# Optimization experiments

Hardware: AMD Instinct MI355X
Metric: run time of the kernel (lower is better)

Reference implementation:

```python
import jax, jax.numpy as jnp
import numpy as np

ALPHA = 4.0  # spikingjelly sigmoid surrogate alpha
EPS = 1e-5   # BatchNorm eps
TAU = 2.0
NUM_HEADS = 8

@jax.custom_vjp
def _spike(x):
    return (x >= 0.0).astype(x.dtype)

def _spike_fwd(x):
    return _spike(x), x

def _spike_bwd(x, g):
    s = jax.nn.sigmoid(ALPHA * x)
    return (g * ALPHA * s * (1.0 - s),)

_spike.defvjp(_spike_fwd, _spike_bwd)

def lif(x, v_th=1.0):
    # MultiStepLIFNode: v += (x - v)/tau, spike = H(v - v_th), hard reset to 0 (detached)
    def step(v, xt):
        v = v + (xt - v) / TAU
        s = _spike(v - v_th)
        v = v * (1.0 - jax.lax.stop_gradient(s))
        return v, s
    _, spikes = jax.lax.scan(step, jnp.zeros_like(x[0]), x)
    return spikes

def bn(x, gamma, beta, mean, var):
    sh = (1, 1, -1, 1, 1)  # channel axis 2 of [T,B,C,H,W]
    inv = gamma.reshape(sh) / jnp.sqrt(var.reshape(sh) + EPS)
    return (x - mean.reshape(sh)) * inv + beta.reshape(sh)

def setup_inputs() -> dict:
    T, B, C, H, W = 4, 16, 384, 32, 32
    key = jax.random.key(0)
    ks = jax.random.split(key, 10)
    def wmat(k):
        return jax.random.normal(k, (C, C), jnp.float32) * 0.05
    def bn_params(k):
        k1, k2, k3, k4 = jax.random.split(k, 4)
        return (jax.random.uniform(k1, (C,), jnp.float32, 0.5, 1.5),
                jax.random.normal(k2, (C,), jnp.float32) * 0.1,
                jax.random.normal(k3, (C,), jnp.float32) * 0.1,
                jax.random.uniform(k4, (C,), jnp.float32, 0.5, 1.5))
    qg, qb, qm, qv = bn_params(ks[2])
    kg, kb, km, kv_ = bn_params(ks[3])
    vg, vb, vm, vv = bn_params(ks[4])
    pg, pb, pm, pv = bn_params(ks[5])
    return {
        'x': jax.random.normal(ks[0], (T, B, C, H, W), jnp.float32),
        'q_w': wmat(ks[1]), 'q_gamma': qg, 'q_beta': qb, 'q_mean': qm, 'q_var': qv,
        'k_w': wmat(ks[6]), 'k_gamma': kg, 'k_beta': kb, 'k_mean': km, 'k_var': kv_,
        'v_w': wmat(ks[7]), 'v_gamma': vg, 'v_beta': vb, 'v_mean': vm, 'v_var': vv,
        'proj_w': wmat(ks[8]), 'proj_b': jax.random.normal(ks[9], (C,), jnp.float32) * 0.02,
        'proj_gamma': pg, 'proj_beta': pb, 'proj_mean': pm, 'proj_var': pv,
    }

def reference(x, q_w, q_gamma, q_beta, q_mean, q_var,
              k_w, k_gamma, k_beta, k_mean, k_var,
              v_w, v_gamma, v_beta, v_mean, v_var,
              proj_w, proj_b, proj_gamma, proj_beta, proj_mean, proj_var):
    T, B, C, H, W = x.shape
    N = H * W
    h = NUM_HEADS
    d = C // h
    identity = x
    xs = lif(x)  # shortcut_lif

    def branch(w_, g_, b_, m_, var_):
        y = jnp.einsum('tbchw,dc->tbdhw', xs, w_)  # conv1x1, no bias
        return lif(bn(y, g_, b_, m_, var_))

    def to_heads(t):  # [T,B,C,H,W] -> [T,B,h,N,d]
        return (t.reshape(T, B, C, N).transpose(0, 1, 3, 2)
                 .reshape(T, B, N, h, d).transpose(0, 1, 3, 2, 4))

    q = to_heads(branch(q_w, q_gamma, q_beta, q_mean, q_var))
    k = to_heads(branch(k_w, k_gamma, k_beta, k_mean, k_var))
    v = to_heads(branch(v_w, v_gamma, v_beta, v_mean, v_var))

    kv = lif((k * v).sum(axis=3, keepdims=True), v_th=0.5)  # [T,B,h,1,d]
    out = q * kv  # [T,B,h,N,d]
    out = out.transpose(0, 1, 2, 4, 3).reshape(T, B, C, H, W)
    out = jnp.einsum('tbchw,dc->tbdhw', out, proj_w) + proj_b.reshape(1, 1, -1, 1, 1)
    out = bn(out, proj_gamma, proj_beta, proj_mean, proj_var)
    return (out + identity, v)
```

## Files before the change

kernel.cpp:

```cpp
#include <hip/hip_runtime.h>
#include <math.h>

#define T_ 4
#define B_ 16
#define C_ 384
#define N_ 1024
#define CN_ (C_ * N_)
#define BCN_ (B_ * CN_)
#define TBCN_ (T_ * BCN_)
#define HEADS_ 8
#define DH_ 48
#define EPS_ 1e-5f
#define NW_ 12
#define M3_ 1152

__global__ __launch_bounds__(256) void prep_wt_qkv(
        const float* __restrict__ qw, const float* __restrict__ kw,
        const float* __restrict__ vw, float* __restrict__ Wt) {
    int idx = blockIdx.x * 256 + threadIdx.x;
    int m = idx / C_, c = idx % C_;
    Wt[(size_t)c * M3_ + m]       = qw[idx];
    Wt[(size_t)c * M3_ + 384 + m] = kw[idx];
    Wt[(size_t)c * M3_ + 768 + m] = vw[idx];
}

__global__ __launch_bounds__(256) void prep_wt_proj(
        const float* __restrict__ pw, float* __restrict__ Wtp) {
    int idx = blockIdx.x * 256 + threadIdx.x;
    int m = idx / C_, c = idx % C_;
    Wtp[(size_t)c * C_ + m] = pw[idx];
}

__global__ __launch_bounds__(256) void prep_bn(
        const float* __restrict__ qg, const float* __restrict__ qb,
        const float* __restrict__ qm, const float* __restrict__ qv,
        const float* __restrict__ kg, const float* __restrict__ kb,
        const float* __restrict__ km, const float* __restrict__ kv2,
        const float* __restrict__ vg, const float* __restrict__ vb,
        const float* __restrict__ vm, const float* __restrict__ vv,
        float* __restrict__ invA, float* __restrict__ muA, float* __restrict__ beA) {
    int i = blockIdx.x * 256 + threadIdx.x;
    if (i >= M3_) return;
    int br = i / C_, c = i % C_;
    const float *g, *bb, *mm, *va;
    if (br == 0)      { g = qg; bb = qb; mm = qm; va = qv; }
    else if (br == 1) { g = kg; bb = kb; mm = km; va = kv2; }
    else              { g = vg; bb = vb; mm = vm; va = vv; }
    invA[i] = g[c] / sqrtf(va[c] + EPS_);
    muA[i]  = mm[c];
    beA[i]  = bb[c];
}

__global__ __launch_bounds__(256) void lif_x_mask(const float* __restrict__ x,
                                                  unsigned* __restrict__ mask_x) {
    int n  = blockIdx.x * 256 + threadIdx.x;
    int cw = blockIdx.y;
    int b  = blockIdx.z;
    unsigned wrd[T_] = {0u, 0u, 0u, 0u};
    const float* xb = x + (size_t)b * CN_ + (size_t)cw * 32 * N_ + n;
#pragma unroll 4
    for (int cb = 0; cb < 32; ++cb) {
        const float* xp = xb + (size_t)cb * N_;
        float v = 0.f;
#pragma unroll
        for (int t = 0; t < T_; ++t) {
            float xt = xp[(size_t)t * BCN_];
            v = v + (xt - v) * 0.5f;
            if (v >= 1.0f) { wrd[t] |= (1u << cb); v = 0.f; }
        }
    }
#pragma unroll
    for (int t = 0; t < T_; ++t)
        mask_x[((size_t)(t * B_ + b) * NW_ + cw) * N_ + n] = wrd[t];
}

__global__ __launch_bounds__(256) void qkv_sparse(
        const unsigned* __restrict__ mask_x, const float* __restrict__ Wt,
        const float* __restrict__ invA, const float* __restrict__ muA,
        const float* __restrict__ beA,
        unsigned* __restrict__ mq, unsigned* __restrict__ mk,
        unsigned* __restrict__ mv) {
    const int lane = threadIdx.x & 63;
    const int col  = threadIdx.x >> 6;
    const int n = blockIdx.x * 4 + col;
    const int b = blockIdx.y;

    float inv[18], mu[18], be[18], vst[18];
#pragma unroll
    for (int j = 0; j < 18; ++j) {
        int m = lane + j * 64;
        inv[j] = invA[m]; mu[j] = muA[m]; be[j] = beA[m];
        vst[j] = 0.f;
    }

    for (int t = 0; t < T_; ++t) {
        float acc[18];
#pragma unroll
        for (int j = 0; j < 18; ++j) acc[j] = 0.f;
        const unsigned* mp = mask_x + (size_t)(t * B_ + b) * NW_ * N_ + n;
        for (int w = 0; w < NW_; ++w) {
            unsigned bits = mp[(size_t)w * N_];
            while (bits) {
                int cb = __builtin_ctz(bits);
                bits &= bits - 1;
                const float* wr = Wt + (size_t)(w * 32 + cb) * M3_ + lane;
#pragma unroll
                for (int j = 0; j < 18; ++j) acc[j] += wr[j * 64];
            }
        }
#pragma unroll
        for (int j = 0; j < 18; ++j) {
            float pre = (acc[j] - mu[j]) * inv[j] + be[j];
            float v2 = vst[j] + (pre - vst[j]) * 0.5f;
            bool s = (v2 >= 1.0f);
            vst[j] = s ? 0.f : v2;
            unsigned long long bal = __ballot(s);
            if (lane == 0) {
                int br = j / 6, wq = (j % 6) * 2;
                unsigned* dst = (br == 0 ? mq : (br == 1 ? mk : mv)) +
                                (size_t)(t * B_ + b) * NW_ * N_ + n;
                dst[(size_t)wq * N_]       = (unsigned)bal;
                dst[(size_t)(wq + 1) * N_] = (unsigned)(bal >> 32);
            }
        }
    }
}

__global__ __launch_bounds__(384) void kv_count(const unsigned* __restrict__ mk,
                                                const unsigned* __restrict__ mv,
                                                int* __restrict__ cnt) {
    int tb = blockIdx.x;
    int w = threadIdx.x >> 5, chunk = threadIdx.x & 31;
    __shared__ int sc[C_];
    if (threadIdx.x < C_) sc[threadIdx.x] = 0;
    __syncthreads();
    const unsigned* kp = mk + ((size_t)tb * NW_ + w) * N_ + chunk * 32;
    const unsigned* vp = mv + ((size_t)tb * NW_ + w) * N_ + chunk * 32;
    int loc[32];
#pragma unroll
    for (int bit = 0; bit < 32; ++bit) loc[bit] = 0;
#pragma unroll
    for (int i = 0; i < 32; ++i) {
        unsigned a = kp[i] & vp[i];
#pragma unroll
        for (int bit = 0; bit < 32; ++bit) loc[bit] += (int)((a >> bit) & 1u);
    }
#pragma unroll
    for (int bit = 0; bit < 32; ++bit)
        if (loc[bit]) atomicAdd(&sc[w * 32 + bit], loc[bit]);
    __syncthreads();
    if (threadIdx.x < C_) cnt[(size_t)tb * C_ + threadIdx.x] = sc[threadIdx.x];
}

__global__ __launch_bounds__(384) void kv_lif(const int* __restrict__ cnt,
                                              unsigned* __restrict__ kvw) {
    int b = blockIdx.x, c = threadIdx.x;
    float u = 0.f;
    for (int t = 0; t < T_; ++t) {
        float ct = (float)cnt[(size_t)(t * B_ + b) * C_ + c];
        u = u + (ct - u) * 0.5f;
        bool s = (u >= 0.5f);
        u = s ? 0.f : u;
        unsigned long long bal = __ballot(s);
        if ((c & 63) == 0) {
            int wv = c >> 6;
            kvw[(size_t)(t * B_ + b) * NW_ + wv * 2]     = (unsigned)bal;
            kvw[(size_t)(t * B_ + b) * NW_ + wv * 2 + 1] = (unsigned)(bal >> 32);
        }
    }
}

__global__ __launch_bounds__(256) void v_to_out1(const unsigned* __restrict__ mv,
                                                 float* __restrict__ out1) {
    int tb = blockIdx.y;
    int n0 = blockIdx.x * 128;
    __shared__ unsigned ws_[NW_][128];
    for (int i = threadIdx.x; i < NW_ * 128; i += 256) {
        int w = i >> 7, nn = i & 127;
        ws_[w][nn] = mv[((size_t)tb * NW_ + w) * N_ + n0 + nn];
    }
    __syncthreads();
    float* dst = out1 + (size_t)tb * HEADS_ * N_ * DH_;
    for (int h = 0; h < HEADS_; ++h) {
        float* dh = dst + ((size_t)h * N_ + n0) * DH_;
#pragma unroll
        for (int l = 0; l < 24; ++l) {
            int flat = l * 256 + threadIdx.x;
            int nn = flat / DH_, dd = flat - nn * DH_;
            int c = h * DH_ + dd;
            unsigned wd = ws_[c >> 5][nn];
            dh[flat] = (float)((wd >> (c & 31)) & 1u);
        }
    }
}

__global__ __launch_bounds__(256) void proj_out0(
        const unsigned* __restrict__ mq, const unsigned* __restrict__ kvw,
        const float* __restrict__ Wtp, const float* __restrict__ pb,
        const float* __restrict__ pg, const float* __restrict__ pbe,
        const float* __restrict__ pm, const float* __restrict__ pv,
        const float* __restrict__ x, float* __restrict__ out0) {
    int tb = blockIdx.y;
    int n0 = blockIdx.x * 64;
    int m0 = blockIdx.z * 128;
    __shared__ float acc[128][65];
    const int lane = threadIdx.x & 63, wv = threadIdx.x >> 6;

    unsigned kvr[NW_];
    const unsigned* kvp = kvw + (size_t)tb * NW_;
#pragma unroll
    for (int w = 0; w < NW_; ++w) kvr[w] = kvp[w];

    for (int ci = 0; ci < 16; ++ci) {
        int coln = wv * 16 + ci;
        const unsigned* mp = mq + (size_t)tb * NW_ * N_ + n0 + coln;
        unsigned bw[NW_];
#pragma unroll
        for (int w = 0; w < NW_; ++w) bw[w] = mp[(size_t)w * N_] & kvr[w];

        float a0 = 0.f, a1 = 0.f, b0 = 0.f, b1 = 0.f;
#pragma unroll
        for (int w = 0; w < NW_; ++w) {
            unsigned bits = bw[w];
            while (bits) {
                int cb0 = __builtin_ctz(bits);
                bits &= bits - 1;
                const float* wr0 = Wtp + (size_t)(w * 32 + cb0) * C_ + m0 + lane;
                if (bits) {
                    int cb1 = __builtin_ctz(bits);
                    bits &= bits - 1;
                    const float* wr1 = Wtp + (size_t)(w * 32 + cb1) * C_ + m0 + lane;
                    float x00 = wr0[0], x01 = wr0[64];
                    float x10 = wr1[0], x11 = wr1[64];
                    a0 += x00; a1 += x01;
                    b0 += x10; b1 += x11;
                } else {
                    a0 += wr0[0];
                    a1 += wr0[64];
                }
            }
        }
        acc[lane][coln]      = a0 + b0;
        acc[lane + 64][coln] = a1 + b1;
    }
    __syncthreads();

    const float* xb = x + (size_t)tb * CN_ + (size_t)m0 * N_ + n0;
    float* ob = out0 + (size_t)tb * CN_ + (size_t)m0 * N_ + n0;
    for (int mi = 0; mi < 32; ++mi) {
        int ml = mi * 4 + wv;
        int m = m0 + ml;
        float inv = pg[m] / sqrtf(pv[m] + EPS_);
        float cst = (pb[m] - pm[m]) * inv + pbe[m];
        float a = acc[ml][lane];
        ob[(size_t)ml * N_ + lane] = a * inv + cst + xb[(size_t)ml * N_ + lane];
    }
}

extern "C" void kernel_launch(void* const* d_in, const int* in_sizes, int n_in,
                              void* d_out, int out_size, void* d_ws, size_t ws_size,
                              hipStream_t stream) {
    (void)in_sizes; (void)n_in; (void)out_size; (void)ws_size;
    const float* x      = (const float*)d_in[0];
    const float* q_w    = (const float*)d_in[1];
    const float* q_g    = (const float*)d_in[2];
    const float* q_b    = (const float*)d_in[3];
    const float* q_m    = (const float*)d_in[4];
    const float* q_v    = (const float*)d_in[5];
    const float* k_w    = (const float*)d_in[6];
    const float* k_g    = (const float*)d_in[7];
    const float* k_b    = (const float*)d_in[8];
    const float* k_m    = (const float*)d_in[9];
    const float* k_v    = (const float*)d_in[10];
    const float* v_w    = (const float*)d_in[11];
    const float* v_g    = (const float*)d_in[12];
    const float* v_b    = (const float*)d_in[13];
    const float* v_m    = (const float*)d_in[14];
    const float* v_v    = (const float*)d_in[15];
    const float* proj_w = (const float*)d_in[16];
    const float* proj_b = (const float*)d_in[17];
    const float* p_g    = (const float*)d_in[18];
    const float* p_be   = (const float*)d_in[19];
    const float* p_m    = (const float*)d_in[20];
    const float* p_v    = (const float*)d_in[21];

    float* out0 = (float*)d_out;
    float* out1 = out0 + TBCN_;

    char* p = (char*)d_ws;
    float* Wt_qkv  = (float*)p;    p += (size_t)C_ * M3_ * 4;
    float* Wt_proj = (float*)p;    p += (size_t)C_ * C_ * 4;
    float* invA    = (float*)p;    p += M3_ * 4;
    float* muA     = (float*)p;    p += M3_ * 4;
    float* beA     = (float*)p;    p += M3_ * 4;
    unsigned* mask_x = (unsigned*)p; p += (size_t)T_ * B_ * NW_ * N_ * 4;
    unsigned* mask_q = (unsigned*)p; p += (size_t)T_ * B_ * NW_ * N_ * 4;
    unsigned* mask_k = (unsigned*)p; p += (size_t)T_ * B_ * NW_ * N_ * 4;
    unsigned* mask_v = (unsigned*)p; p += (size_t)T_ * B_ * NW_ * N_ * 4;
    int* cnt       = (int*)p;      p += (size_t)T_ * B_ * C_ * 4;
    unsigned* kvw  = (unsigned*)p; p += (size_t)T_ * B_ * NW_ * 4;

    prep_wt_qkv<<<(C_ * C_) / 256, 256, 0, stream>>>(q_w, k_w, v_w, Wt_qkv);
    prep_wt_proj<<<(C_ * C_) / 256, 256, 0, stream>>>(proj_w, Wt_proj);
    prep_bn<<<(M3_ + 255) / 256, 256, 0, stream>>>(q_g, q_b, q_m, q_v,
                                                   k_g, k_b, k_m, k_v,
                                                   v_g, v_b, v_m, v_v,
                                                   invA, muA, beA);

    lif_x_mask<<<dim3(N_ / 256, NW_, B_), 256, 0, stream>>>(x, mask_x);

    qkv_sparse<<<dim3(N_ / 4, B_), 256, 0, stream>>>(mask_x, Wt_qkv,
                                                     invA, muA, beA,
                                                     mask_q, mask_k, mask_v);

    kv_count<<<T_ * B_, 384, 0, stream>>>(mask_k, mask_v, cnt);
    kv_lif<<<B_, 384, 0, stream>>>(cnt, kvw);

    v_to_out1<<<dim3(N_ / 128, T_ * B_), 256, 0, stream>>>(mask_v, out1);

    proj_out0<<<dim3(N_ / 64, T_ * B_, 3), 256, 0, stream>>>(
        mask_q, kvw, Wt_proj, proj_b, p_g, p_be, p_m, p_v, x, out0);
}
```

Measured before the change: 569.4 us.

## Vectorize qkv_sparse weight-row loads and permute the spike-mask bit layout to match

Each lane in qkv_sparse now loads float4/float2 slices of a weight row instead of 18 strided scalars. Because of this, the output channels owned by each lane move to contiguous groups, so the ballot-produced mask words take a permuted channel-to-bit mapping. Downstream consumers (v_to_out1 decoding and the proj weight transpose) are rewritten to use the new bit layout. The kernel also preloads mask words, uses readfirstlane to keep the bit loop scalar, processes two set bits per iteration for more memory-level parallelism, and sets an occupancy hint of 4. The risk is bit-mapping errors in consumers not shown, such as kv_count, which indexes bits per channel.

```diff
diff --git a/kernel.cpp b/kernel.cpp
--- a/kernel.cpp
+++ b/kernel.cpp
@@ -14,6 +14,10 @@
 #define NW_ 12
 #define M3_ 1152
 
+typedef float f4 __attribute__((ext_vector_type(4)));
+typedef float f2 __attribute__((ext_vector_type(2)));
+
+
 __global__ __launch_bounds__(256) void prep_wt_qkv(
         const float* __restrict__ qw, const float* __restrict__ kw,
         const float* __restrict__ vw, float* __restrict__ Wt) {
@@ -27,8 +31,11 @@
 __global__ __launch_bounds__(256) void prep_wt_proj(
         const float* __restrict__ pw, float* __restrict__ Wtp) {
     int idx = blockIdx.x * 256 + threadIdx.x;
-    int m = idx / C_, c = idx % C_;
-    Wtp[(size_t)c * C_ + m] = pw[idx];
+    int r = idx / C_, m = idx % C_;
+    int Wb = r >> 5, i = r & 31;
+    int c = (Wb < 8) ? (128 * (Wb & 1) + 4 * i + (Wb >> 1))
+                     : (256 + 4 * i + (Wb - 8));
+    Wtp[(size_t)r * C_ + m] = pw[(size_t)m * C_ + c];
 }
 
 __global__ __launch_bounds__(256) void prep_bn(
@@ -74,7 +81,7 @@
         mask_x[((size_t)(t * B_ + b) * NW_ + cw) * N_ + n] = wrd[t];
 }
 
-__global__ __launch_bounds__(256) void qkv_sparse(
+__global__ __launch_bounds__(256, 4) void qkv_sparse(
         const unsigned* __restrict__ mask_x, const float* __restrict__ Wt,
         const float* __restrict__ invA, const float* __restrict__ muA,
         const float* __restrict__ beA,
@@ -85,42 +92,99 @@
     const int n = blockIdx.x * 4 + col;
     const int b = blockIdx.y;
 
-    float inv[18], mu[18], be[18], vst[18];
-#pragma unroll
-    for (int j = 0; j < 18; ++j) {
-        int m = lane + j * 64;
-        inv[j] = invA[m]; mu[j] = muA[m]; be[j] = beA[m];
-        vst[j] = 0.f;
-    }
+    f4 vs[4] = {f4{0.f,0.f,0.f,0.f}, f4{0.f,0.f,0.f,0.f},
+                f4{0.f,0.f,0.f,0.f}, f4{0.f,0.f,0.f,0.f}};
+    f2 vs4 = f2{0.f, 0.f};
 
     for (int t = 0; t < T_; ++t) {
-        float acc[18];
-#pragma unroll
-        for (int j = 0; j < 18; ++j) acc[j] = 0.f;
-        const unsigned* mp = mask_x + (size_t)(t * B_ + b) * NW_ * N_ + n;
+        const size_t base = (size_t)(t * B_ + b) * NW_ * N_ + n;
+        const unsigned* mp = mask_x + base;
+        unsigned bwv[NW_];
+#pragma unroll
+        for (int w = 0; w < NW_; ++w) bwv[w] = mp[(size_t)w * N_];
+
+        f4 acc[4] = {f4{0.f,0.f,0.f,0.f}, f4{0.f,0.f,0.f,0.f},
+                     f4{0.f,0.f,0.f,0.f}, f4{0.f,0.f,0.f,0.f}};
+        f2 acc4 = f2{0.f, 0.f};
+
         for (int w = 0; w < NW_; ++w) {
-            unsigned bits = mp[(size_t)w * N_];
+            unsigned bits = __builtin_amdgcn_readfirstlane(bwv[w]);
+            const float* wb0 = Wt + (size_t)(w * 32) * M3_;
             while (bits) {
-                int cb = __builtin_ctz(bits);
-                bits &= bits - 1;
-                const float* wr = Wt + (size_t)(w * 32 + cb) * M3_ + lane;
-#pragma unroll
-                for (int j = 0; j < 18; ++j) acc[j] += wr[j * 64];
+                int cb0 = __builtin_ctz(bits); bits &= bits - 1;
+                const float* r0 = wb0 + (size_t)cb0 * M3_;
+                f4 d00 = *(const f4*)(r0 + 4 * lane);
+                f4 d01 = *(const f4*)(r0 + 256 + 4 * lane);
+                f4 d02 = *(const f4*)(r0 + 512 + 4 * lane);
+                f4 d03 = *(const f4*)(r0 + 768 + 4 * lane);
+                f2 d04 = *(const f2*)(r0 + 1024 + 2 * lane);
+                if (bits) {
+                    int cb1 = __builtin_ctz(bits); bits &= bits - 1;
+                    const float* r1 = wb0 + (size_t)cb1 * M3_;
+                    f4 d10 = *(const f4*)(r1 + 4 * lane);
+                    f4 d11 = *(const f4*)(r1 + 256 + 4 * lane);
+                    f4 d12 = *(const f4*)(r1 + 512 + 4 * lane);
+                    f4 d13 = *(const f4*)(r1 + 768 + 4 * lane);
+                    f2 d14 = *(const f2*)(r1 + 1024 + 2 * lane);
+                    acc[0] += d00; acc[1] += d01; acc[2] += d02; acc[3] += d03;
+                    acc4 += d04;
+                    acc[0] += d10; acc[1] += d11; acc[2] += d12; acc[3] += d13;
+                    acc4 += d14;
+                } else {
+                    acc[0] += d00; acc[1] += d01; acc[2] += d02; acc[3] += d03;
+                    acc4 += d04;
+                }
             }
         }
-#pragma unroll
-        for (int j = 0; j < 18; ++j) {
-            float pre = (acc[j] - mu[j]) * inv[j] + be[j];
-            float v2 = vst[j] + (pre - vst[j]) * 0.5f;
-            bool s = (v2 >= 1.0f);
-            vst[j] = s ? 0.f : v2;
-            unsigned long long bal = __ballot(s);
-            if (lane == 0) {
-                int br = j / 6, wq = (j % 6) * 2;
-                unsigned* dst = (br == 0 ? mq : (br == 1 ? mk : mv)) +
-                                (size_t)(t * B_ + b) * NW_ * N_ + n;
-                dst[(size_t)wq * N_]       = (unsigned)bal;
-                dst[(size_t)(wq + 1) * N_] = (unsigned)(bal >> 32);
+
+        unsigned* dq = mq + base;
+        unsigned* dk = mk + base;
+        unsigned* dv = mv + base;
+#pragma unroll
+        for (int g = 0; g < 4; ++g) {
+            f4 iv = *(const f4*)(invA + g * 256 + 4 * lane);
+            f4 mu = *(const f4*)(muA + g * 256 + 4 * lane);
+            f4 be = *(const f4*)(beA + g * 256 + 4 * lane);
+            f4 pre = (acc[g] - mu) * iv + be;
+            f4 v2 = vs[g] + (pre - vs[g]) * 0.5f;
+#pragma unroll
+            for (int q = 0; q < 4; ++q) {
+                bool s = (v2[q] >= 1.0f);
+                vs[g][q] = s ? 0.f : v2[q];
+                unsigned long long bal = __ballot(s);
+                if (lane == 0) {
+                    unsigned lo = (unsigned)bal, hi = (unsigned)(bal >> 32);
+                    if (g == 0) {
+                        dq[(size_t)(2 * q) * N_] = lo;
+                        dq[(size_t)(2 * q + 1) * N_] = hi;
+                    } else if (g == 1) {
+                        dq[(size_t)(8 + q) * N_] = lo;
+                        dk[(size_t)q * N_] = hi;
+                    } else if (g == 2) {
+                        dk[(size_t)(4 + 2 * q) * N_] = lo;
+                        dk[(size_t)(5 + 2 * q) * N_] = hi;
+                    } else {
+                        dv[(size_t)(2 * q) * N_] = lo;
+                        dv[(size_t)(2 * q + 1) * N_] = hi;
+                    }
+                }
+            }
+        }
+        {
+            f2 iv = *(const f2*)(invA + 1024 + 2 * lane);
+            f2 mu = *(const f2*)(muA + 1024 + 2 * lane);
+            f2 be = *(const f2*)(beA + 1024 + 2 * lane);
+            f2 pre = (acc4 - mu) * iv + be;
+            f2 v2 = vs4 + (pre - vs4) * 0.5f;
+#pragma unroll
+            for (int q = 0; q < 2; ++q) {
+                bool s = (v2[q] >= 1.0f);
+                vs4[q] = s ? 0.f : v2[q];
+                unsigned long long bal = __ballot(s);
+                if (lane == 0) {
+                    dv[(size_t)(8 + 2 * q) * N_] = (unsigned)bal;
+                    dv[(size_t)(9 + 2 * q) * N_] = (unsigned)(bal >> 32);
+                }
             }
         }
     }
@@ -188,8 +252,11 @@
             int flat = l * 256 + threadIdx.x;
             int nn = flat / DH_, dd = flat - nn * DH_;
             int c = h * DH_ + dd;
-            unsigned wd = ws_[c >> 5][nn];
-            dh[flat] = (float)((wd >> (c & 31)) & 1u);
+            int Wb, bit;
+            if (c < 256) { Wb = 2 * (c & 3) + (c >> 7); bit = (c & 127) >> 2; }
+            else { int r = c - 256; Wb = 8 + 2 * (r & 1) + (r >> 6); bit = (r & 63) >> 1; }
+            unsigned wd = ws_[Wb][nn];
+            dh[flat] = (float)((wd >> bit) & 1u);
         }
     }
 }
```

Result: slower. 648.6 us (+13.9%).

## Split qkv_sparse per branch with vectorized weight loads and permuted channel bit layout

Applied to the files above, without the earlier changes.

The sparse QKV kernel now runs one branch per grid z-slice. Each lane loads 4+2 contiguous weight floats as vector loads instead of 18 scalar strided loads, and the spike-bit loop is unrolled by four using a wave-uniform mask read via readfirstlane. Because each lane now owns contiguous channels, the output bitmask words use a permuted channel-to-bit mapping, and v_to_out1 and the projection weight transpose are rewritten to match. The mask_x reads are repeated three times across the split grid, in exchange for better memory coalescing and more parallelism.

```diff
diff --git a/kernel.cpp b/kernel.cpp
--- a/kernel.cpp
+++ b/kernel.cpp
@@ -14,6 +14,10 @@
 #define NW_ 12
 #define M3_ 1152
 
+typedef float f4 __attribute__((ext_vector_type(4)));
+typedef float f2 __attribute__((ext_vector_type(2)));
+
+
 __global__ __launch_bounds__(256) void prep_wt_qkv(
         const float* __restrict__ qw, const float* __restrict__ kw,
         const float* __restrict__ vw, float* __restrict__ Wt) {
@@ -27,8 +31,11 @@
 __global__ __launch_bounds__(256) void prep_wt_proj(
         const float* __restrict__ pw, float* __restrict__ Wtp) {
     int idx = blockIdx.x * 256 + threadIdx.x;
-    int m = idx / C_, c = idx % C_;
-    Wtp[(size_t)c * C_ + m] = pw[idx];
+    int r = idx / C_, m = idx % C_;
+    int Wb = r >> 5, i = r & 31;
+    int c = (Wb < 8) ? (128 * (Wb & 1) + 4 * i + (Wb >> 1))
+                     : (256 + 64 * ((Wb - 8) & 1) + 2 * i + ((Wb - 8) >> 1));
+    Wtp[(size_t)r * C_ + m] = pw[(size_t)m * C_ + c];
 }
 
 __global__ __launch_bounds__(256) void prep_bn(
@@ -84,43 +91,87 @@
     const int col  = threadIdx.x >> 6;
     const int n = blockIdx.x * 4 + col;
     const int b = blockIdx.y;
-
-    float inv[18], mu[18], be[18], vst[18];
-#pragma unroll
-    for (int j = 0; j < 18; ++j) {
-        int m = lane + j * 64;
-        inv[j] = invA[m]; mu[j] = muA[m]; be[j] = beA[m];
-        vst[j] = 0.f;
-    }
+    const int br = blockIdx.z;
+
+    const int cb4 = 4 * lane;
+    const int cb2 = 256 + 2 * lane;
+    const int boff = br * C_;
+
+    f4 iv4 = *(const f4*)(invA + boff + cb4);
+    f4 mu4 = *(const f4*)(muA + boff + cb4);
+    f4 be4 = *(const f4*)(beA + boff + cb4);
+    f2 iv2 = *(const f2*)(invA + boff + cb2);
+    f2 mu2 = *(const f2*)(muA + boff + cb2);
+    f2 be2 = *(const f2*)(beA + boff + cb2);
+
+    unsigned* dst0 = (br == 0 ? mq : (br == 1 ? mk : mv));
+
+    f4 vs4_ = f4{0.f, 0.f, 0.f, 0.f};
+    f2 vs2_ = f2{0.f, 0.f};
 
     for (int t = 0; t < T_; ++t) {
-        float acc[18];
-#pragma unroll
-        for (int j = 0; j < 18; ++j) acc[j] = 0.f;
-        const unsigned* mp = mask_x + (size_t)(t * B_ + b) * NW_ * N_ + n;
+        const size_t base = (size_t)(t * B_ + b) * NW_ * N_ + n;
+        const unsigned* mp = mask_x + base;
+        unsigned bwv[NW_];
+#pragma unroll
+        for (int w = 0; w < NW_; ++w) bwv[w] = mp[(size_t)w * N_];
+
+        f4 a4 = f4{0.f, 0.f, 0.f, 0.f};
+        f2 a2 = f2{0.f, 0.f};
+
         for (int w = 0; w < NW_; ++w) {
-            unsigned bits = mp[(size_t)w * N_];
-            while (bits) {
-                int cb = __builtin_ctz(bits);
-                bits &= bits - 1;
-                const float* wr = Wt + (size_t)(w * 32 + cb) * M3_ + lane;
-#pragma unroll
-                for (int j = 0; j < 18; ++j) acc[j] += wr[j * 64];
-            }
-        }
-#pragma unroll
-        for (int j = 0; j < 18; ++j) {
-            float pre = (acc[j] - mu[j]) * inv[j] + be[j];
-            float v2 = vst[j] + (pre - vst[j]) * 0.5f;
-            bool s = (v2 >= 1.0f);
-            vst[j] = s ? 0.f : v2;
+            unsigned bits = __builtin_amdgcn_readfirstlane(bwv[w]);
+            const float* wb0 = Wt + (size_t)(w * 32) * M3_ + boff;
+            int np = __builtin_popcount(bits);
+            for (; np >= 4; np -= 4) {
+                int c0 = __builtin_ctz(bits); bits &= bits - 1;
+                int c1 = __builtin_ctz(bits); bits &= bits - 1;
+                int c2 = __builtin_ctz(bits); bits &= bits - 1;
+                int c3 = __builtin_ctz(bits); bits &= bits - 1;
+                const float* r0 = wb0 + (size_t)c0 * M3_;
+                const float* r1 = wb0 + (size_t)c1 * M3_;
+                const float* r2 = wb0 + (size_t)c2 * M3_;
+                const float* r3 = wb0 + (size_t)c3 * M3_;
+                f4 x0 = *(const f4*)(r0 + cb4); f2 y0 = *(const f2*)(r0 + cb2);
+                f4 x1 = *(const f4*)(r1 + cb4); f2 y1 = *(const f2*)(r1 + cb2);
+                f4 x2 = *(const f4*)(r2 + cb4); f2 y2 = *(const f2*)(r2 + cb2);
+                f4 x3 = *(const f4*)(r3 + cb4); f2 y3 = *(const f2*)(r3 + cb2);
+                a4 += x0; a2 += y0;
+                a4 += x1; a2 += y1;
+                a4 += x2; a2 += y2;
+                a4 += x3; a2 += y3;
+            }
+            for (; np > 0; --np) {
+                int c0 = __builtin_ctz(bits); bits &= bits - 1;
+                const float* r0 = wb0 + (size_t)c0 * M3_;
+                f4 x0 = *(const f4*)(r0 + cb4); f2 y0 = *(const f2*)(r0 + cb2);
+                a4 += x0; a2 += y0;
+            }
+        }
+
+        unsigned* d = dst0 + base;
+        f4 pre4 = (a4 - mu4) * iv4 + be4;
+        f4 v24 = vs4_ + (pre4 - vs4_) * 0.5f;
+#pragma unroll
+        for (int q = 0; q < 4; ++q) {
+            bool s = (v24[q] >= 1.0f);
+            vs4_[q] = s ? 0.f : v24[q];
             unsigned long long bal = __ballot(s);
             if (lane == 0) {
-                int br = j / 6, wq = (j % 6) * 2;
-                unsigned* dst = (br == 0 ? mq : (br == 1 ? mk : mv)) +
-                                (size_t)(t * B_ + b) * NW_ * N_ + n;
-                dst[(size_t)wq * N_]       = (unsigned)bal;
-                dst[(size_t)(wq + 1) * N_] = (unsigned)(bal >> 32);
+                d[(size_t)(2 * q) * N_]     = (unsigned)bal;
+                d[(size_t)(2 * q + 1) * N_] = (unsigned)(bal >> 32);
+            }
+        }
+        f2 pre2 = (a2 - mu2) * iv2 + be2;
+        f2 v22 = vs2_ + (pre2 - vs2_) * 0.5f;
+#pragma unroll
+        for (int q = 0; q < 2; ++q) {
+            bool s = (v22[q] >= 1.0f);
+            vs2_[q] = s ? 0.f : v22[q];
+            unsigned long long bal = __ballot(s);
+            if (lane == 0) {
+                d[(size_t)(8 + 2 * q) * N_] = (unsigned)bal;
+                d[(size_t)(9 + 2 * q) * N_] = (unsigned)(bal >> 32);
             }
         }
     }
@@ -188,8 +239,11 @@
             int flat = l * 256 + threadIdx.x;
             int nn = flat / DH_, dd = flat - nn * DH_;
             int c = h * DH_ + dd;
-            unsigned wd = ws_[c >> 5][nn];
-            dh[flat] = (float)((wd >> (c & 31)) & 1u);
+            int Wb, bit;
+            if (c < 256) { Wb = 2 * (c & 3) + (c >> 7); bit = (c & 127) >> 2; }
+            else { int r = c - 256; Wb = 8 + 2 * (r & 1) + (r >> 6); bit = (r & 63) >> 1; }
+            unsigned wd = ws_[Wb][nn];
+            dh[flat] = (float)((wd >> bit) & 1u);
         }
     }
 }
@@ -309,9 +363,9 @@
 
     lif_x_mask<<<dim3(N_ / 256, NW_, B_), 256, 0, stream>>>(x, mask_x);
 
-    qkv_sparse<<<dim3(N_ / 4, B_), 256, 0, stream>>>(mask_x, Wt_qkv,
-                                                     invA, muA, beA,
-                                                     mask_q, mask_k, mask_v);
+    qkv_sparse<<<dim3(N_ / 4, B_, 3), 256, 0, stream>>>(mask_x, Wt_qkv,
+                                                        invA, muA, beA,
+                                                        mask_q, mask_k, mask_v);
 
     kv_count<<<T_ * B_, 384, 0, stream>>>(mask_k, mask_v, cnt);
     kv_lif<<<B_, 384, 0, stream>>>(cnt, kvw);
```

New measurement: 602.1 us. 1.06x slower.
